# Kernel tuning notes

Hardware: AMD Instinct MI355X
Metric: run time of the kernel (lower is better)

The kernel has to match this reference:

```python
import jax, jax.numpy as jnp
import numpy as np

B, T, C = 2, 2048, 2048
NH, NKV = 16, 4
HD = C // NH  # 128


def _rope(x, cos, sin):
    d = x.shape[-1] // 2
    x1, x2 = x[..., :d], x[..., d:]
    return jnp.concatenate([x1 * cos + x2 * sin, -x1 * sin + x2 * cos], axis=-1)


def _rmsnorm(x):
    eps = jnp.finfo(x.dtype).eps
    return x * jax.lax.rsqrt(jnp.mean(jnp.square(x), axis=-1, keepdims=True) + eps)


def setup_inputs() -> dict:
    key = jax.random.key(0)
    ks = jax.random.split(key, 7)
    s = 0.02
    return {
        "x": jax.random.normal(ks[0], (B, T, C), jnp.float32),
        "cos": jax.random.normal(ks[1], (1, T, 1, HD // 2), jnp.float32),
        "sin": jax.random.normal(ks[2], (1, T, 1, HD // 2), jnp.float32),
        "wq": jax.random.normal(ks[3], (C, NH * HD), jnp.float32) * s,
        "wk": jax.random.normal(ks[4], (C, NKV * HD), jnp.float32) * s,
        "wv": jax.random.normal(ks[5], (C, NKV * HD), jnp.float32) * s,
        "wo": jax.random.normal(ks[6], (C, C), jnp.float32) * s,
    }


def reference(x, cos, sin, wq, wk, wv, wo):
    q = (x @ wq).reshape(B, T, NH, HD)
    k = (x @ wk).reshape(B, T, NKV, HD)
    v = (x @ wv).reshape(B, T, NKV, HD)
    q = _rmsnorm(_rope(q, cos, sin))
    k = _rmsnorm(_rope(k, cos, sin))
    # [B, H, T, D]
    q = q.transpose(0, 2, 1, 3)
    k = k.transpose(0, 2, 1, 3)
    v = v.transpose(0, 2, 1, 3)
    rep = NH // NKV
    k = jnp.repeat(k, rep, axis=1)
    v = jnp.repeat(v, rep, axis=1)
    scale = 1.0 / jnp.sqrt(jnp.float32(HD))
    scores = jnp.einsum("bhqd,bhkd->bhqk", q, k) * scale
    causal = jnp.tril(jnp.ones((T, T), bool))
    scores = jnp.where(causal, scores, jnp.finfo(scores.dtype).min)
    attn = jax.nn.softmax(scores, axis=-1)
    y = jnp.einsum("bhqk,bhkd->bhqd", attn, v)
    y = y.transpose(0, 2, 1, 3).reshape(B, T, C)
    return y @ wo
```

## Files before the change

### kernel.cpp

```cpp
#include <hip/hip_runtime.h>
#include <hip/hip_bf16.h>
#include <cstdint>

typedef unsigned short u16;
typedef __bf16 bf16x8 __attribute__((ext_vector_type(8)));
typedef float f32x4 __attribute__((ext_vector_type(4)));
typedef unsigned short u16x4 __attribute__((ext_vector_type(4)));
typedef unsigned uint2v __attribute__((ext_vector_type(2)));

#define B_ 2
#define T_ 2048
#define C_ 2048
#define NH_ 16
#define NKV_ 4
#define HD_ 128
#define K2_ 0.12752004650581538f

__device__ __forceinline__ u16 f2bf(float f) {
    unsigned u = __builtin_bit_cast(unsigned, f);
    unsigned r = u + 0x7FFFu + ((u >> 16) & 1u);
    return (u16)(r >> 16);
}

__device__ __forceinline__ unsigned cvtpk(float a, float b) {
    unsigned r;
    asm("v_cvt_pk_bf16_f32 %0, %1, %2" : "=v"(r) : "v"(a), "v"(b));
    return r;
}

__device__ __forceinline__ void gl16(const void* g, void* l) {
    auto gp = reinterpret_cast<const __attribute__((address_space(1))) unsigned*>(
        reinterpret_cast<uintptr_t>(g));
    auto lp = reinterpret_cast<__attribute__((address_space(3))) unsigned*>(
        reinterpret_cast<uintptr_t>(l));
    __builtin_amdgcn_global_load_lds(gp, lp, 16, 0, 0);
}

__global__ void transpose_conv(const float* __restrict__ in, u16* __restrict__ out, int N) {
    __shared__ float tile[32][33];
    int n0 = blockIdx.x * 32, k0 = blockIdx.y * 32;
    int tx = threadIdx.x, ty = threadIdx.y;
#pragma unroll
    for (int i = 0; i < 4; ++i)
        tile[ty * 4 + i][tx] = in[(size_t)(k0 + ty * 4 + i) * N + n0 + tx];
    __syncthreads();
#pragma unroll
    for (int i = 0; i < 4; ++i)
        out[(size_t)(n0 + ty * 4 + i) * 2048 + k0 + tx] = f2bf(tile[tx][ty * 4 + i]);
}

__global__ void convert4(const float4* __restrict__ in, u16* __restrict__ out) {
    int i = blockIdx.x * 256 + threadIdx.x;
    float4 v = in[i];
    u16x4 o;
    o[0] = f2bf(v.x); o[1] = f2bf(v.y); o[2] = f2bf(v.z); o[3] = f2bf(v.w);
    ((u16x4*)out)[i] = o;
}

__global__ __launch_bounds__(256, 2) void gemm_bf16(const u16* __restrict__ A,
                                                    const u16* __restrict__ BT,
                                                    float* __restrict__ C, int N, int K) {
    __shared__ __align__(16) u16 As[128 * 64];
    __shared__ __align__(16) u16 Bs[128 * 64];
    int nwg = gridDim.x * gridDim.y;
    int bid = blockIdx.y * gridDim.x + blockIdx.x;
    int nb = (bid & 7) * (nwg >> 3) + (bid >> 3);
    int bx = nb % gridDim.x, by = nb / gridDim.x;

    int t = threadIdx.x;
    int w = t >> 6, l = t & 63;
    int wr = w >> 1, wc = w & 1;
    int lg = l >> 4, lr = l & 15;
    int m0 = by * 128, n0 = bx * 128;
    f32x4 acc[4][4] = {};
    int ar = t >> 3;
    int acb = (t & 7) * 16;
    const char* Abase = (const char*)(A + (size_t)(m0 + ar) * K) + acb;
    const char* Bbase = (const char*)(BT + (size_t)(n0 + ar) * K) + acb;
    char* AsB = (char*)As + t * 16;
    char* BsB = (char*)Bs + t * 16;
    for (int kt = 0; kt < K; kt += 64) {
        if (kt) __syncthreads();
#pragma unroll
        for (int i = 0; i < 4; ++i) {
            gl16(Abase + (size_t)(i * 32) * K * 2 + (size_t)kt * 2, AsB + i * 4096);
            gl16(Bbase + (size_t)(i * 32) * K * 2 + (size_t)kt * 2, BsB + i * 4096);
        }
        __syncthreads();
#pragma unroll
        for (int kk = 0; kk < 2; ++kk) {
            bf16x8 af[4], bfr[4];
#pragma unroll
            for (int m = 0; m < 4; ++m)
                af[m] = *(const bf16x8*)(As + (wr * 64 + m * 16 + lr) * 64 + kk * 32 + lg * 8);
#pragma unroll
            for (int n = 0; n < 4; ++n)
                bfr[n] = *(const bf16x8*)(Bs + (wc * 64 + n * 16 + lr) * 64 + kk * 32 + lg * 8);
#pragma unroll
            for (int m = 0; m < 4; ++m)
#pragma unroll
                for (int n = 0; n < 4; ++n)
                    acc[m][n] = __builtin_amdgcn_mfma_f32_16x16x32_bf16(af[m], bfr[n], acc[m][n], 0, 0, 0);
        }
    }
#pragma unroll
    for (int m = 0; m < 4; ++m) {
        int row = m0 + wr * 64 + m * 16 + lg * 4;
#pragma unroll
        for (int n = 0; n < 4; ++n) {
            int col = n0 + wc * 64 + n * 16 + lr;
            float* Cp = C + (size_t)row * N + col;
#pragma unroll
            for (int r = 0; r < 4; ++r)
                Cp[(size_t)r * N] = acc[m][n][r];
        }
    }
}

__global__ void rope_rms(const float* __restrict__ qkv, const float* __restrict__ cs,
                         const float* __restrict__ sn, u16* __restrict__ qh,
                         u16* __restrict__ kh) {
    int task = blockIdx.x * 4 + (threadIdx.x >> 6);
    int l = threadIdx.x & 63;
    const float* in;
    u16* out;
    int tpos;
    float post = 1.0f;
    if (task < 65536) {
        int row = task >> 4, h = task & 15;
        in = qkv + (size_t)row * 3072 + h * 128;
        int b = row >> 11; tpos = row & 2047;
        out = qh + ((size_t)(b * NH_ + h) * T_ + tpos) * HD_;
        post = K2_;
    } else {
        int t2 = task - 65536;
        int row = t2 >> 2, h = t2 & 3;
        in = qkv + (size_t)row * 3072 + 2048 + h * 128;
        int b = row >> 11; tpos = row & 2047;
        out = kh + ((size_t)(b * NKV_ + h) * T_ + tpos) * HD_;
    }
    float x1 = in[l], x2 = in[l + 64];
    float c = cs[tpos * 64 + l], s = sn[tpos * 64 + l];
    float o1 = x1 * c + x2 * s;
    float o2 = -x1 * s + x2 * c;
    float ss = o1 * o1 + o2 * o2;
#pragma unroll
    for (int m = 1; m < 64; m <<= 1) ss += __shfl_xor(ss, m);
    float r = rsqrtf(ss * (1.0f / 128.0f) + 1.1920929e-07f) * post;
    out[l] = f2bf(o1 * r);
    out[l + 64] = f2bf(o2 * r);
}

__global__ void transpose_v(const float* __restrict__ qkv, u16* __restrict__ vt) {
    __shared__ float tile[32][33];
    int t0 = blockIdx.x * 32;
    int d0 = blockIdx.y * 32;
    int bk = blockIdx.z;
    int b = bk >> 2, kvh = bk & 3;
    int tx = threadIdx.x, ty = threadIdx.y;
#pragma unroll
    for (int i = 0; i < 4; ++i)
        tile[ty * 4 + i][tx] =
            qkv[(size_t)(b * 2048 + t0 + ty * 4 + i) * 3072 + 2560 + kvh * 128 + d0 + tx];
    __syncthreads();
#pragma unroll
    for (int i = 0; i < 4; ++i)
        vt[((size_t)bk * 128 + d0 + ty * 4 + i) * 2048 + t0 + tx] = f2bf(tile[tx][ty * 4 + i]);
}

__global__ __launch_bounds__(256, 2) void attn(const u16* __restrict__ Q,
                                               const u16* __restrict__ Kk,
                                               const u16* __restrict__ V,
                                               u16* __restrict__ Y) {
    extern __shared__ __align__(16) u16 sm[];
    u16* Ks = sm;
    u16* Vs = sm + 16384;
    u16* Pb = sm + 32768;

    int bid = blockIdx.x;
    int xcd = bid & 7;
    int b = xcd >> 2, kvh = xcd & 3;
    int j = bid >> 3;
    int t = threadIdx.x;
    int w = t >> 6, l = t & 63;
    int lg = l >> 4, lr = l & 15;
    int h = kvh * 4 + w;
    int qwA = j * 16, qwB = (127 - j) * 16;
    int NA = j / 4 + 1;

    const u16* Qp = Q + (size_t)(b * NH_ + h) * T_ * HD_;
    const u16* Kp = Kk + (size_t)(b * NKV_ + kvh) * T_ * HD_;
    const u16* Vp = V + (size_t)(b * NKV_ + kvh) * HD_ * T_;
    u16* Yp = Y + (size_t)(b * T_) * 2048 + h * HD_;
    u16* Pw = Pb + w * 1152;

    auto stage = [&](int kv0, int buf) {
        const char* Kb = (const char*)Kp + (size_t)kv0 * 256;
        const char* Vb = (const char*)Vp + (size_t)kv0 * 2;
        char* Kd = (char*)(Ks + buf * 8192);
        char* Vd = (char*)(Vs + buf * 8192);
#pragma unroll
        for (int i = 0; i < 4; ++i) {
            int g = t + i * 256;
            gl16(Kb + (g >> 4) * 256 + (((g & 15) ^ ((g >> 4) & 15)) * 16), Kd + g * 16);
            gl16(Vb + (size_t)(g >> 3) * 4096 + (((g & 7) ^ ((g >> 3) & 7)) * 16), Vd + g * 16);
        }
    };

    bf16x8 aq[4];
    auto loadQ = [&](int qw2) {
#pragma unroll
        for (int ch = 0; ch < 4; ++ch)
            aq[ch] = *(const bf16x8*)(Qp + (size_t)(qw2 + lr) * HD_ + ch * 32 + lg * 8);
    };

    f32x4 acc[8] = {};
    float m2 = -1e30f, lpS = 0.0f;

    auto epi = [&](int qw2) {
        float lt = lpS;
        lt += __shfl_xor(lt, 16);
        lt += __shfl_xor(lt, 32);
        float inv = 1.0f / lt;
        float inv4[4];
#pragma unroll
        for (int r = 0; r < 4; ++r) inv4[r] = __shfl(inv, 4 * lg + r, 16);
#pragma unroll
        for (int oc = 0; oc < 8; ++oc)
#pragma unroll
            for (int r = 0; r < 4; ++r)
                Yp[(size_t)(qw2 + 4 * lg + r) * 2048 + oc * 16 + lr] = f2bf(acc[oc][r] * inv4[r]);
    };

    loadQ(qwA);
    int qw = qwA;
    stage(0, 0);

    for (int gi = 0; gi < 33; ++gi) {
        asm volatile("s_waitcnt vmcnt(0)" ::: "memory");
        __builtin_amdgcn_s_barrier();
        __builtin_amdgcn_sched_barrier(0);
        int cur = gi & 1;
        if (gi < 32) {
            int gn = gi + 1;
            stage((gn < NA ? gn : gn - NA) * 64, cur ^ 1);
        }
        if (gi == NA) {
            epi(qwA);
#pragma unroll
            for (int oc = 0; oc < 8; ++oc) acc[oc] = f32x4{0.f, 0.f, 0.f, 0.f};
            m2 = -1e30f; lpS = 0.0f;
            loadQ(qwB);
            qw = qwB;
        }
        int kv0 = (gi < NA ? gi : gi - NA) * 64;
        int kbase = cur * 8192;

        f32x4 sc[4] = {};
        __builtin_amdgcn_s_setprio(1);
#pragma unroll
        for (int ch = 0; ch < 4; ++ch)
#pragma unroll
            for (int kf = 0; kf < 4; ++kf) {
                bf16x8 bk = *(const bf16x8*)&Ks[kbase + (kf * 16 + lr) * 128 + (((ch * 4 + lg) ^ lr) * 8)];
                sc[kf] = __builtin_amdgcn_mfma_f32_16x16x32_bf16(bk, aq[ch], sc[kf], 0, 0, 0);
            }
        __builtin_amdgcn_s_setprio(0);

        int qrow = qw + lr;
        bool nm = (kv0 + 63 > qw);
        if (nm) {
#pragma unroll
            for (int kf = 0; kf < 4; ++kf)
#pragma unroll
                for (int r = 0; r < 4; ++r) {
                    int key = kv0 + kf * 16 + 4 * lg + r;
                    if (key > qrow) sc[kf][r] = -1e38f;
                }
        }
        float mk[4];
#pragma unroll
        for (int kf = 0; kf < 4; ++kf)
            mk[kf] = fmaxf(fmaxf(sc[kf][0], sc[kf][1]), fmaxf(sc[kf][2], sc[kf][3]));
        float mx = fmaxf(fmaxf(mk[0], mk[1]), fmaxf(mk[2], mk[3]));
        mx = fmaxf(mx, __shfl_xor(mx, 16));
        mx = fmaxf(mx, __shfl_xor(mx, 32));

        if (__any(mx > m2 + 8.0f)) {
            float mn = fmaxf(m2, mx);
            float rs = exp2f(m2 - mn);
            m2 = mn;
            lpS *= rs;
            float rs4[4];
#pragma unroll
            for (int r = 0; r < 4; ++r) rs4[r] = __shfl(rs, 4 * lg + r, 16);
#pragma unroll
            for (int oc = 0; oc < 8; ++oc)
#pragma unroll
                for (int r = 0; r < 4; ++r) acc[oc][r] *= rs4[r];
        }

        float ps = 0.0f;
#pragma unroll
        for (int kf = 0; kf < 4; ++kf) {
            float p0 = exp2f(sc[kf][0] - m2);
            float p1 = exp2f(sc[kf][1] - m2);
            float p2 = exp2f(sc[kf][2] - m2);
            float p3 = exp2f(sc[kf][3] - m2);
            ps += (p0 + p1) + (p2 + p3);
            uint2v pk;
            pk[0] = cvtpk(p0, p1);
            pk[1] = cvtpk(p2, p3);
            *(uint2v*)&Pw[lr * 72 + kf * 16 + 4 * lg] = pk;
        }
        lpS += ps;

        bf16x8 ap[2];
#pragma unroll
        for (int kk = 0; kk < 2; ++kk)
            ap[kk] = *(const bf16x8*)&Pw[lr * 72 + kk * 32 + 8 * lg];
        __builtin_amdgcn_s_setprio(1);
#pragma unroll
        for (int oc = 0; oc < 8; ++oc)
#pragma unroll
            for (int kk = 0; kk < 2; ++kk) {
                bf16x8 bv = *(const bf16x8*)&Vs[kbase + (oc * 16 + lr) * 64 +
                                                (((kk * 4 + lg) ^ (lr & 7)) * 8)];
                acc[oc] = __builtin_amdgcn_mfma_f32_16x16x32_bf16(ap[kk], bv, acc[oc], 0, 0, 0);
            }
        __builtin_amdgcn_s_setprio(0);
    }
    epi(qwB);
}

extern "C" void kernel_launch(void* const* d_in, const int* in_sizes, int n_in,
                              void* d_out, int out_size, void* d_ws, size_t ws_size,
                              hipStream_t stream) {
    const float* x    = (const float*)d_in[0];
    const float* cosT = (const float*)d_in[1];
    const float* sinT = (const float*)d_in[2];
    const float* wq   = (const float*)d_in[3];
    const float* wk   = (const float*)d_in[4];
    const float* wv   = (const float*)d_in[5];
    const float* wo   = (const float*)d_in[6];
    float* out = (float*)d_out;

    char* ws = (char*)d_ws;
    u16*   wqkvT = (u16*)(ws);
    u16*   woT   = (u16*)(ws + 12582912);
    u16*   xb    = (u16*)(ws + 20971520);
    float* qkv   = (float*)(ws + 37748736);
    u16*   qh    = (u16*)(ws + 88080384);
    u16*   kh    = (u16*)(ws + 104857600);
    u16*   vt    = (u16*)(ws + 109051904);
    u16*   y     = xb;

    hipFuncSetAttribute(reinterpret_cast<const void*>(&attn),
                        hipFuncAttributeMaxDynamicSharedMemorySize, 74752);

    transpose_conv<<<dim3(64, 64), dim3(32, 8), 0, stream>>>(wq, wqkvT, 2048);
    transpose_conv<<<dim3(16, 64), dim3(32, 8), 0, stream>>>(wk, wqkvT + (size_t)2048 * 2048, 512);
    transpose_conv<<<dim3(16, 64), dim3(32, 8), 0, stream>>>(wv, wqkvT + (size_t)2560 * 2048, 512);
    transpose_conv<<<dim3(64, 64), dim3(32, 8), 0, stream>>>(wo, woT, 2048);
    convert4<<<8192, 256, 0, stream>>>((const float4*)x, xb);

    gemm_bf16<<<dim3(24, 32), 256, 0, stream>>>(xb, wqkvT, qkv, 3072, 2048);

    rope_rms<<<20480, 256, 0, stream>>>(qkv, cosT, sinT, qh, kh);
    transpose_v<<<dim3(64, 4, 8), dim3(32, 8), 0, stream>>>(qkv, vt);

    attn<<<512, 256, 74752, stream>>>(qh, kh, vt, y);

    gemm_bf16<<<dim3(16, 32), 256, 0, stream>>>(y, woT, out, 2048, 2048);
}
```

Baseline: 225.6 us.

## Process two 16-row Q tiles per wave, schedule causal blocks longest-first

Each wave now handles 32 query rows (two 16-row fragments), so every K and V fragment read from LDS feeds two MFMAs. This replaces the earlier scheme of pairing a short and a long 16-row tile per block for load balance. Work balance now comes from launching the blocks with the most causal KV iterations first. It also precomputes the per-thread staging offsets and uses a swizzled P buffer in LDS. In exchange, register pressure roughly doubles for the accumulators and scores, LDS grows, and per-block work is uneven, which relies on the scheduler's tail behaviour.

Measured after the change: 224.4 us. Within noise of the previous version (-0.6%).

```diff
diff --git a/kernel.cpp b/kernel.cpp
--- a/kernel.cpp
+++ b/kernel.cpp
@@ -180,45 +180,155 @@
     int bid = blockIdx.x;
     int xcd = bid & 7;
     int b = xcd >> 2, kvh = xcd & 3;
-    int j = bid >> 3;
+    int q = bid >> 3;
+    int j = (q < 32) ? (63 - q) : (q - 32);
+    int NN = (j >> 1) + 1;
     int t = threadIdx.x;
     int w = t >> 6, l = t & 63;
     int lg = l >> 4, lr = l & 15;
     int h = kvh * 4 + w;
-    int qwA = j * 16, qwB = (127 - j) * 16;
-    int NA = j / 4 + 1;
+    int qw = j * 32;
 
     const u16* Qp = Q + (size_t)(b * NH_ + h) * T_ * HD_;
     const u16* Kp = Kk + (size_t)(b * NKV_ + kvh) * T_ * HD_;
     const u16* Vp = V + (size_t)(b * NKV_ + kvh) * HD_ * T_;
     u16* Yp = Y + (size_t)(b * T_) * 2048 + h * HD_;
-    u16* Pw = Pb + w * 1152;
-
+    u16* Pw = Pb + w * 2048;
+
+    size_t koff[4], voff[4];
+#pragma unroll
+    for (int i = 0; i < 4; ++i) {
+        int g = t + i * 256;
+        koff[i] = (size_t)(g >> 4) * 256 + (size_t)(((g & 15) ^ ((g >> 4) & 15)) * 16);
+        voff[i] = (size_t)(g >> 3) * (T_ * 2) + (size_t)(((g & 7) ^ ((g >> 3) & 7)) * 16);
+    }
     auto stage = [&](int kv0, int buf) {
         const char* Kb = (const char*)Kp + (size_t)kv0 * 256;
         const char* Vb = (const char*)Vp + (size_t)kv0 * 2;
-        char* Kd = (char*)(Ks + buf * 8192);
-        char* Vd = (char*)(Vs + buf * 8192);
+        char* Kd = (char*)Ks + buf * 16384 + t * 16;
+        char* Vd = (char*)Vs + buf * 16384 + t * 16;
 #pragma unroll
         for (int i = 0; i < 4; ++i) {
-            int g = t + i * 256;
-            gl16(Kb + (g >> 4) * 256 + (((g & 15) ^ ((g >> 4) & 15)) * 16), Kd + g * 16);
-            gl16(Vb + (size_t)(g >> 3) * 4096 + (((g & 7) ^ ((g >> 3) & 7)) * 16), Vd + g * 16);
+            gl16(Kb + koff[i], Kd + i * 4096);
+            gl16(Vb + voff[i], Vd + i * 4096);
         }
     };
 
-    bf16x8 aq[4];
-    auto loadQ = [&](int qw2) {
+    bf16x8 aq[2][4];
+#pragma unroll
+    for (int qf = 0; qf < 2; ++qf)
 #pragma unroll
         for (int ch = 0; ch < 4; ++ch)
-            aq[ch] = *(const bf16x8*)(Qp + (size_t)(qw2 + lr) * HD_ + ch * 32 + lg * 8);
-    };
-
-    f32x4 acc[8] = {};
-    float m2 = -1e30f, lpS = 0.0f;
-
-    auto epi = [&](int qw2) {
-        float lt = lpS;
+            aq[qf][ch] = *(const bf16x8*)(Qp + (size_t)(qw + qf * 16 + lr) * HD_ + ch * 32 + lg * 8);
+
+    f32x4 acc[2][8] = {};
+    float m2[2] = {-1e30f, -1e30f};
+    float lp_[2] = {0.0f, 0.0f};
+
+    stage(0, 0);
+
+    for (int gi = 0; gi < NN; ++gi) {
+        asm volatile("s_waitcnt vmcnt(0)" ::: "memory");
+        __builtin_amdgcn_s_barrier();
+        __builtin_amdgcn_sched_barrier(0);
+        int cur = gi & 1;
+        if (gi + 1 < NN) stage((gi + 1) * 64, cur ^ 1);
+        int kv0 = gi * 64;
+        int kbase = cur * 8192;
+
+        f32x4 sc[2][4] = {};
+        __builtin_amdgcn_s_setprio(1);
+#pragma unroll
+        for (int ch = 0; ch < 4; ++ch)
+#pragma unroll
+            for (int kf = 0; kf < 4; ++kf) {
+                bf16x8 bk = *(const bf16x8*)&Ks[kbase + (kf * 16 + lr) * 128 + (((ch * 4 + lg) ^ lr) * 8)];
+                sc[0][kf] = __builtin_amdgcn_mfma_f32_16x16x32_bf16(bk, aq[0][ch], sc[0][kf], 0, 0, 0);
+                sc[1][kf] = __builtin_amdgcn_mfma_f32_16x16x32_bf16(bk, aq[1][ch], sc[1][kf], 0, 0, 0);
+            }
+        __builtin_amdgcn_s_setprio(0);
+
+        if (kv0 + 63 > qw) {
+#pragma unroll
+            for (int qf = 0; qf < 2; ++qf) {
+                int qrow = qw + qf * 16 + lr;
+#pragma unroll
+                for (int kf = 0; kf < 4; ++kf)
+#pragma unroll
+                    for (int r = 0; r < 4; ++r) {
+                        int key = kv0 + kf * 16 + 4 * lg + r;
+                        if (key > qrow) sc[qf][kf][r] = -1e38f;
+                    }
+            }
+        }
+        float mx[2];
+#pragma unroll
+        for (int qf = 0; qf < 2; ++qf) {
+            float m = sc[qf][0][0];
+#pragma unroll
+            for (int kf = 0; kf < 4; ++kf)
+#pragma unroll
+                for (int r = 0; r < 4; ++r) m = fmaxf(m, sc[qf][kf][r]);
+            m = fmaxf(m, __shfl_xor(m, 16));
+            m = fmaxf(m, __shfl_xor(m, 32));
+            mx[qf] = m;
+        }
+        bool upd = (mx[0] > m2[0] + 8.0f) || (mx[1] > m2[1] + 8.0f);
+        if (__any(upd)) {
+#pragma unroll
+            for (int qf = 0; qf < 2; ++qf) {
+                float mn = fmaxf(m2[qf], mx[qf]);
+                float rs = exp2f(m2[qf] - mn);
+                m2[qf] = mn;
+                lp_[qf] *= rs;
+                float rs4[4];
+#pragma unroll
+                for (int r = 0; r < 4; ++r) rs4[r] = __shfl(rs, 4 * lg + r, 16);
+#pragma unroll
+                for (int oc = 0; oc < 8; ++oc)
+#pragma unroll
+                    for (int r = 0; r < 4; ++r) acc[qf][oc][r] *= rs4[r];
+            }
+        }
+#pragma unroll
+        for (int qf = 0; qf < 2; ++qf) {
+            float ps = 0.0f;
+#pragma unroll
+            for (int kf = 0; kf < 4; ++kf) {
+                float p0 = exp2f(sc[qf][kf][0] - m2[qf]);
+                float p1 = exp2f(sc[qf][kf][1] - m2[qf]);
+                float p2 = exp2f(sc[qf][kf][2] - m2[qf]);
+                float p3 = exp2f(sc[qf][kf][3] - m2[qf]);
+                ps += (p0 + p1) + (p2 + p3);
+                uint2v pk;
+                pk[0] = cvtpk(p0, p1);
+                pk[1] = cvtpk(p2, p3);
+                int g16 = 2 * kf + (lg >> 1);
+                *(uint2v*)&Pw[(qf * 16 + lr) * 64 + ((g16 ^ (lr & 7)) * 8) + (lg & 1) * 4] = pk;
+            }
+            lp_[qf] += ps;
+        }
+        bf16x8 ap[2][2];
+#pragma unroll
+        for (int qf = 0; qf < 2; ++qf)
+#pragma unroll
+            for (int kk = 0; kk < 2; ++kk)
+                ap[qf][kk] = *(const bf16x8*)&Pw[(qf * 16 + lr) * 64 + (((4 * kk + lg) ^ (lr & 7)) * 8)];
+        __builtin_amdgcn_s_setprio(1);
+#pragma unroll
+        for (int oc = 0; oc < 8; ++oc)
+#pragma unroll
+            for (int kk = 0; kk < 2; ++kk) {
+                bf16x8 bv = *(const bf16x8*)&Vs[kbase + (oc * 16 + lr) * 64 +
+                                                (((kk * 4 + lg) ^ (lr & 7)) * 8)];
+                acc[0][oc] = __builtin_amdgcn_mfma_f32_16x16x32_bf16(ap[0][kk], bv, acc[0][oc], 0, 0, 0);
+                acc[1][oc] = __builtin_amdgcn_mfma_f32_16x16x32_bf16(ap[1][kk], bv, acc[1][oc], 0, 0, 0);
+            }
+        __builtin_amdgcn_s_setprio(0);
+    }
+#pragma unroll
+    for (int qf = 0; qf < 2; ++qf) {
+        float lt = lp_[qf];
         lt += __shfl_xor(lt, 16);
         lt += __shfl_xor(lt, 32);
         float inv = 1.0f / lt;
@@ -229,108 +339,9 @@
         for (int oc = 0; oc < 8; ++oc)
 #pragma unroll
             for (int r = 0; r < 4; ++r)
-                Yp[(size_t)(qw2 + 4 * lg + r) * 2048 + oc * 16 + lr] = f2bf(acc[oc][r] * inv4[r]);
-    };
-
-    loadQ(qwA);
-    int qw = qwA;
-    stage(0, 0);
-
-    for (int gi = 0; gi < 33; ++gi) {
-        asm volatile("s_waitcnt vmcnt(0)" ::: "memory");
-        __builtin_amdgcn_s_barrier();
-        __builtin_amdgcn_sched_barrier(0);
-        int cur = gi & 1;
-        if (gi < 32) {
-            int gn = gi + 1;
-            stage((gn < NA ? gn : gn - NA) * 64, cur ^ 1);
-        }
-        if (gi == NA) {
-            epi(qwA);
-#pragma unroll
-            for (int oc = 0; oc < 8; ++oc) acc[oc] = f32x4{0.f, 0.f, 0.f, 0.f};
-            m2 = -1e30f; lpS = 0.0f;
-            loadQ(qwB);
-            qw = qwB;
-        }
-        int kv0 = (gi < NA ? gi : gi - NA) * 64;
-        int kbase = cur * 8192;
-
-        f32x4 sc[4] = {};
-        __builtin_amdgcn_s_setprio(1);
-#pragma unroll
-        for (int ch = 0; ch < 4; ++ch)
-#pragma unroll
-            for (int kf = 0; kf < 4; ++kf) {
-                bf16x8 bk = *(const bf16x8*)&Ks[kbase + (kf * 16 + lr) * 128 + (((ch * 4 + lg) ^ lr) * 8)];
-                sc[kf] = __builtin_amdgcn_mfma_f32_16x16x32_bf16(bk, aq[ch], sc[kf], 0, 0, 0);
-            }
-        __builtin_amdgcn_s_setprio(0);
-
-        int qrow = qw + lr;
-        bool nm = (kv0 + 63 > qw);
-        if (nm) {
-#pragma unroll
-            for (int kf = 0; kf < 4; ++kf)
-#pragma unroll
-                for (int r = 0; r < 4; ++r) {
-                    int key = kv0 + kf * 16 + 4 * lg + r;
-                    if (key > qrow) sc[kf][r] = -1e38f;
-                }
-        }
-        float mk[4];
-#pragma unroll
-        for (int kf = 0; kf < 4; ++kf)
-            mk[kf] = fmaxf(fmaxf(sc[kf][0], sc[kf][1]), fmaxf(sc[kf][2], sc[kf][3]));
-        float mx = fmaxf(fmaxf(mk[0], mk[1]), fmaxf(mk[2], mk[3]));
-        mx = fmaxf(mx, __shfl_xor(mx, 16));
-        mx = fmaxf(mx, __shfl_xor(mx, 32));
-
-        if (__any(mx > m2 + 8.0f)) {
-            float mn = fmaxf(m2, mx);
-            float rs = exp2f(m2 - mn);
-            m2 = mn;
-            lpS *= rs;
-            float rs4[4];
-#pragma unroll
-            for (int r = 0; r < 4; ++r) rs4[r] = __shfl(rs, 4 * lg + r, 16);
-#pragma unroll
-            for (int oc = 0; oc < 8; ++oc)
-#pragma unroll
-                for (int r = 0; r < 4; ++r) acc[oc][r] *= rs4[r];
-        }
-
-        float ps = 0.0f;
-#pragma unroll
-        for (int kf = 0; kf < 4; ++kf) {
-            float p0 = exp2f(sc[kf][0] - m2);
-            float p1 = exp2f(sc[kf][1] - m2);
-            float p2 = exp2f(sc[kf][2] - m2);
-            float p3 = exp2f(sc[kf][3] - m2);
-            ps += (p0 + p1) + (p2 + p3);
-            uint2v pk;
-            pk[0] = cvtpk(p0, p1);
-            pk[1] = cvtpk(p2, p3);
-            *(uint2v*)&Pw[lr * 72 + kf * 16 + 4 * lg] = pk;
-        }
-        lpS += ps;
-
-        bf16x8 ap[2];
-#pragma unroll
-        for (int kk = 0; kk < 2; ++kk)
-            ap[kk] = *(const bf16x8*)&Pw[lr * 72 + kk * 32 + 8 * lg];
-        __builtin_amdgcn_s_setprio(1);
-#pragma unroll
-        for (int oc = 0; oc < 8; ++oc)
-#pragma unroll
-            for (int kk = 0; kk < 2; ++kk) {
-                bf16x8 bv = *(const bf16x8*)&Vs[kbase + (oc * 16 + lr) * 64 +
-                                                (((kk * 4 + lg) ^ (lr & 7)) * 8)];
-                acc[oc] = __builtin_amdgcn_mfma_f32_16x16x32_bf16(ap[kk], bv, acc[oc], 0, 0, 0);
-            }
-        __builtin_amdgcn_s_setprio(0);
-    }
-    epi(qwB);
+                Yp[(size_t)(qw + qf * 16 + 4 * lg + r) * 2048 + oc * 16 + lr] =
+                    f2bf(acc[qf][oc][r] * inv4[r]);
+    }
 }
 
 extern "C" void kernel_launch(void* const* d_in, const int* in_sizes, int n_in,
@@ -356,7 +367,7 @@
     u16*   y     = xb;
 
     hipFuncSetAttribute(reinterpret_cast<const void*>(&attn),
-                        hipFuncAttributeMaxDynamicSharedMemorySize, 74752);
+                        hipFuncAttributeMaxDynamicSharedMemorySize, 81920);
 
     transpose_conv<<<dim3(64, 64), dim3(32, 8), 0, stream>>>(wq, wqkvT, 2048);
     transpose_conv<<<dim3(16, 64), dim3(32, 8), 0, stream>>>(wk, wqkvT + (size_t)2048 * 2048, 512);
@@ -369,7 +380,7 @@
     rope_rms<<<20480, 256, 0, stream>>>(qkv, cosT, sinT, qh, kh);
     transpose_v<<<dim3(64, 4, 8), dim3(32, 8), 0, stream>>>(qkv, vt);
 
-    attn<<<512, 256, 74752, stream>>>(qh, kh, vt, y);
+    attn<<<512, 256, 81920, stream>>>(qh, kh, vt, y);
 
     gemm_bf16<<<dim3(16, 32), 256, 0, stream>>>(y, woT, out, 2048, 2048);
 }
```
